# Kernel tuning notes

Hardware: AMD Instinct MI355X
Metric: run time of the kernel (lower is better)

Reference implementation:

```python
import jax, jax.numpy as jnp
import numpy as np

NEG_SLOPE = 0.2  # DenseGATConv default negative_slope


def dense_gat(x, adj, W, att_src, att_dst, bias):
    # x: [B,N,Cin], adj: [B,N,N] (self-loops already added), W: [Cin,H*C]
    B, N, _ = x.shape
    H, C = att_src.shape
    h = (x @ W).reshape(B, N, H, C)
    a_src = jnp.einsum('bnhc,hc->bnh', h, att_src)  # [B,N,H]
    a_dst = jnp.einsum('bnhc,hc->bnh', h, att_dst)
    # alpha[b,i,j,h] = a_src[b,j,h] + a_dst[b,i,h]  (softmax over j, axis=2)
    alpha = a_src[:, None, :, :] + a_dst[:, :, None, :]
    alpha = jnp.where(alpha >= 0, alpha, NEG_SLOPE * alpha)  # leaky_relu
    mask = (adj != 0)[..., None]  # [B,N,N,1]
    alpha = jax.nn.softmax(jnp.where(mask, alpha, -1e30), axis=2)
    out = jnp.einsum('bijh,bjhc->bihc', alpha, h).reshape(B, N, H * C)
    return out + bias


def setup_inputs() -> dict:
    key = jax.random.key(0)
    ks = jax.random.split(key, 8)
    B, N, D = 1, 8192, 128
    x = jax.random.normal(ks[0], (B, N, D), dtype=jnp.float32)
    adj = (jax.random.uniform(ks[1], (B, N, N)) < 0.01).astype(jnp.float32)
    idx = jnp.arange(N)
    adj = adj.at[:, idx, idx].set(1.0)  # DenseGATConv add_loop=True
    s = 1.0 / np.sqrt(D)
    lin = lambda k: jax.random.uniform(k, (D, D), minval=-s, maxval=s, dtype=jnp.float32)
    att = lambda k: jax.random.normal(k, (1, D), dtype=jnp.float32) * 0.1  # heads=1
    return dict(
        x=x, adj=adj,
        W0=lin(ks[2]), att_src0=att(ks[3]), att_dst0=att(ks[4]), b0=jnp.zeros((D,), jnp.float32),
        W1=lin(ks[5]), att_src1=att(ks[6]), att_dst1=att(ks[7]), b1=jnp.zeros((D,), jnp.float32),
    )


def reference(x, adj, W0, att_src0, att_dst0, b0, W1, att_src1, att_dst1, b1):
    out0 = dense_gat(x, adj, W0, att_src0, att_dst0, b0)
    out0 = jax.nn.relu(out0)  # relu_layers_index = [0]
    out1 = dense_gat(out0, adj, W1, att_src1, att_dst1, b1)
    # dropout_rate = 0 -> dropout is identity; squeeze batch dim as in block
    return (out0[0], out1[0])
```

## Files before the change

### kernel.cpp

```cpp
#include <hip/hip_runtime.h>

#define MAXDEG 192
#define NEG_SLOPE 0.2f
#define D 128

__device__ __forceinline__ float bf2f(unsigned short u) {
    return __uint_as_float(((unsigned)u) << 16);
}
__device__ __forceinline__ unsigned short f2bf(float f) {
    unsigned u = __float_as_uint(f);
    return (unsigned short)((u + 0x7fffu + ((u >> 16) & 1u)) >> 16);
}
__device__ __forceinline__ int is_f32(const void* adj) {
    return ((const unsigned*)adj)[0] == 0x3F800000u;
}

__device__ __forceinline__ void ell_group(
        int g, const void* __restrict__ adj, int N, int f32m,
        unsigned short* __restrict__ cols, int* __restrict__ deg,
        int* __restrict__ cnt ) {
    const int w = threadIdx.x >> 6, lane = threadIdx.x & 63;
    const int row = g * 4 + w;
    if (lane == 0) cnt[w] = 0;
    __syncthreads();
    unsigned short* crow = cols + (size_t)row * MAXDEG;
    if (f32m) {
        const float4* arow = (const float4*)((const float*)adj + (size_t)row * N);
        const int nv = N / 4;
        for (int v = lane; v < nv; v += 128) {
            float4 u0 = arow[v];
            float4 u1 = arow[v + 64];
            const unsigned* a0 = (const unsigned*)&u0;
            const unsigned* a1 = (const unsigned*)&u1;
            #pragma unroll
            for (int e = 0; e < 4; e++)
                if (a0[e]) { int p = atomicAdd(&cnt[w], 1); if (p < MAXDEG) crow[p] = (unsigned short)(v * 4 + e); }
            #pragma unroll
            for (int e = 0; e < 4; e++)
                if (a1[e]) { int p = atomicAdd(&cnt[w], 1); if (p < MAXDEG) crow[p] = (unsigned short)((v + 64) * 4 + e); }
        }
    } else {
        const uint4* arow = (const uint4*)((const unsigned short*)adj + (size_t)row * N);
        const int nv = N / 8;
        for (int v = lane; v < nv; v += 128) {
            uint4 u0 = arow[v];
            uint4 u1 = arow[v + 64];
            const unsigned short* s0 = (const unsigned short*)&u0;
            const unsigned short* s1 = (const unsigned short*)&u1;
            #pragma unroll
            for (int e = 0; e < 8; e++)
                if (s0[e]) { int p = atomicAdd(&cnt[w], 1); if (p < MAXDEG) crow[p] = (unsigned short)(v * 8 + e); }
            #pragma unroll
            for (int e = 0; e < 8; e++)
                if (s1[e]) { int p = atomicAdd(&cnt[w], 1); if (p < MAXDEG) crow[p] = (unsigned short)((v + 64) * 8 + e); }
        }
    }
    __syncthreads();
    if (lane == 0) deg[row] = cnt[w] < MAXDEG ? cnt[w] : MAXDEG;
}

__device__ __forceinline__ void gemm_tile(
        int t, const void* __restrict__ A, const void* __restrict__ W,
        int aF, int f32m, const void* __restrict__ attS, const void* __restrict__ attD,
        float* __restrict__ H, float* __restrict__ asrc, float* __restrict__ adst,
        float* __restrict__ smem) {
    float* xs = smem;
    float* ws = smem + 4096;
    const int tid = threadIdx.x;
    const size_t row0 = (size_t)t * 32;

    if (aF) {
        const float4* av = (const float4*)((const float*)A + row0 * D);
        float4* xl = (float4*)xs;
        #pragma unroll
        for (int k = 0; k < 4; k++) xl[tid + 256 * k] = av[tid + 256 * k];
    } else {
        const uint4* av = (const uint4*)((const unsigned short*)A + row0 * D);
        #pragma unroll
        for (int k = 0; k < 2; k++) {
            uint4 u = av[tid + 256 * k];
            const unsigned short* us = (const unsigned short*)&u;
            #pragma unroll
            for (int e = 0; e < 8; e++) xs[(tid + 256 * k) * 8 + e] = bf2f(us[e]);
        }
    }

    const int tx = tid & 31, ty = tid >> 5;
    const int c0 = tx * 4, r0 = ty * 4;
    float acc[4][4] = {};
    for (int p = 0; p < 4; p++) {
        __syncthreads();
        if (f32m) {
            const float4* wv = (const float4*)((const float*)W + (size_t)p * 32 * D);
            float4* wl = (float4*)ws;
            #pragma unroll
            for (int k = 0; k < 4; k++) wl[tid + 256 * k] = wv[tid + 256 * k];
        } else {
            const uint4* wv = (const uint4*)((const unsigned short*)W + (size_t)p * 32 * D);
            #pragma unroll
            for (int k = 0; k < 2; k++) {
                uint4 u = wv[tid + 256 * k];
                const unsigned short* us = (const unsigned short*)&u;
                #pragma unroll
                for (int e = 0; e < 8; e++) ws[(tid + 256 * k) * 8 + e] = bf2f(us[e]);
            }
        }
        __syncthreads();
        #pragma unroll 8
        for (int k = 0; k < 32; k++) {
            float4 wv = *(const float4*)&ws[k * D + c0];
            #pragma unroll
            for (int i = 0; i < 4; i++) {
                float xv = xs[(r0 + i) * D + p * 32 + k];
                acc[i][0] += xv * wv.x; acc[i][1] += xv * wv.y;
                acc[i][2] += xv * wv.z; acc[i][3] += xv * wv.w;
            }
        }
    }
    float* Ho = H + row0 * D;
    #pragma unroll
    for (int i = 0; i < 4; i++)
        *(float4*)&Ho[(r0 + i) * D + c0] =
            make_float4(acc[i][0], acc[i][1], acc[i][2], acc[i][3]);

    float aSv[4], aDv[4];
    #pragma unroll
    for (int j = 0; j < 4; j++) {
        aSv[j] = f32m ? ((const float*)attS)[c0 + j] : bf2f(((const unsigned short*)attS)[c0 + j]);
        aDv[j] = f32m ? ((const float*)attD)[c0 + j] : bf2f(((const unsigned short*)attD)[c0 + j]);
    }
    #pragma unroll
    for (int i = 0; i < 4; i++) {
        float s = acc[i][0] * aSv[0] + acc[i][1] * aSv[1] + acc[i][2] * aSv[2] + acc[i][3] * aSv[3];
        float d = acc[i][0] * aDv[0] + acc[i][1] * aDv[1] + acc[i][2] * aDv[2] + acc[i][3] * aDv[3];
        #pragma unroll
        for (int off = 16; off > 0; off >>= 1) {
            s += __shfl_down(s, off, 32);
            d += __shfl_down(d, off, 32);
        }
        if (tx == 0) {
            asrc[row0 + r0 + i] = s;
            adst[row0 + r0 + i] = d;
        }
    }
}

__global__ __launch_bounds__(256) void ell_gemm0(
        const void* __restrict__ x, const void* __restrict__ adj,
        const void* __restrict__ W0, const void* __restrict__ aS0,
        const void* __restrict__ aD0, int N,
        unsigned short* __restrict__ cols, int* __restrict__ deg,
        float* __restrict__ h, float* __restrict__ asrc, float* __restrict__ adst) {
    __shared__ float smem[8192];
    const int bid = blockIdx.x;
    const int f32m = is_f32(adj);
    const int GT = N / 32;
    if (bid < GT)
        gemm_tile(bid, x, W0, f32m, f32m, aS0, aD0, h, asrc, adst, smem);
    else
        ell_group(bid - GT, adj, N, f32m, cols, deg, (int*)smem);
}

__global__ __launch_bounds__(256) void aggregate(
        const float* __restrict__ H,
        const float* __restrict__ asrc, const float* __restrict__ adst,
        const unsigned short* __restrict__ cols, const int* __restrict__ deg,
        const void* __restrict__ bias, const void* __restrict__ adjFlag,
        float* __restrict__ outF, void* __restrict__ outAny,
        size_t off2, int relu) {
    __shared__ float scnA[4 * MAXDEG];
    __shared__ unsigned short sjjA[4 * MAXDEG];
    const int w = threadIdx.x >> 6, lane = threadIdx.x & 63;
    const int row = blockIdx.x * 4 + w;
    float* scn = scnA + w * MAXDEG;
    unsigned short* sjj = sjjA + w * MAXDEG;
    const int d = deg[row];
    const float ai = adst[row];
    const unsigned short* crow = cols + (size_t)row * MAXDEG;

    const int s0 = lane, s1 = lane + 64, s2 = lane + 128;
    unsigned short j0 = 0, j1 = 0, j2 = 0;
    float e0 = -3e38f, e1 = -3e38f, e2 = -3e38f;
    if (s0 < d) { j0 = crow[s0]; float e = asrc[j0] + ai; e0 = (e >= 0.f) ? e : NEG_SLOPE * e; }
    if (s1 < d) { j1 = crow[s1]; float e = asrc[j1] + ai; e1 = (e >= 0.f) ? e : NEG_SLOPE * e; }
    if (s2 < d) { j2 = crow[s2]; float e = asrc[j2] + ai; e2 = (e >= 0.f) ? e : NEG_SLOPE * e; }
    float m = fmaxf(e0, fmaxf(e1, e2));
    #pragma unroll
    for (int off = 1; off < 64; off <<= 1) m = fmaxf(m, __shfl_xor(m, off));
    float p0 = (s0 < d) ? __expf(e0 - m) : 0.f;
    float p1 = (s1 < d) ? __expf(e1 - m) : 0.f;
    float p2 = (s2 < d) ? __expf(e2 - m) : 0.f;
    float l = p0 + p1 + p2;
    #pragma unroll
    for (int off = 1; off < 64; off <<= 1) l += __shfl_xor(l, off);
    const float invl = 1.f / l;
    scn[s0] = p0 * invl; sjj[s0] = j0;
    scn[s1] = p1 * invl; sjj[s1] = j1;
    scn[s2] = p2 * invl; sjj[s2] = j2;

    const float2* H2 = (const float2*)H;
    float2 acc[8];
    #pragma unroll
    for (int u = 0; u < 8; u++) acc[u] = make_float2(0.f, 0.f);
    int k = 0;
    for (; k + 7 < d; k += 8) {
        int jj[8]; float ww[8]; float2 vv[8];
        #pragma unroll
        for (int u = 0; u < 8; u++) { jj[u] = sjj[k + u]; ww[u] = scn[k + u]; }
        #pragma unroll
        for (int u = 0; u < 8; u++) vv[u] = H2[(size_t)jj[u] * 64 + lane];
        #pragma unroll
        for (int u = 0; u < 8; u++) { acc[u].x += ww[u] * vv[u].x; acc[u].y += ww[u] * vv[u].y; }
    }
    for (; k < d; k++) {
        const int j = sjj[k];
        const float wk = scn[k];
        const float2 v = H2[(size_t)j * 64 + lane];
        acc[0].x += wk * v.x; acc[0].y += wk * v.y;
    }
    #pragma unroll
    for (int u = 1; u < 8; u++) { acc[0].x += acc[u].x; acc[0].y += acc[u].y; }
    float vx = acc[0].x, vy = acc[0].y;

    const int f32m = is_f32(adjFlag);
    const int c0 = lane * 2;
    const float bx = f32m ? ((const float*)bias)[c0]     : bf2f(((const unsigned short*)bias)[c0]);
    const float by = f32m ? ((const float*)bias)[c0 + 1] : bf2f(((const unsigned short*)bias)[c0 + 1]);
    vx += bx; vy += by;
    if (relu) { vx = fmaxf(vx, 0.f); vy = fmaxf(vy, 0.f); }
    if (outF) ((float2*)outF)[(size_t)row * 64 + lane] = make_float2(vx, vy);
    if (f32m) {
        ((float2*)outAny)[off2 + (size_t)row * 64 + lane] = make_float2(vx, vy);
    } else {
        unsigned packed = (unsigned)f2bf(vx) | ((unsigned)f2bf(vy) << 16);
        ((unsigned*)outAny)[off2 + (size_t)row * 64 + lane] = packed;
    }
}

__global__ __launch_bounds__(256) void gemm1(
        const float* __restrict__ A, const void* __restrict__ W1,
        const void* __restrict__ aS1, const void* __restrict__ aD1,
        const void* __restrict__ adjFlag,
        float* __restrict__ h, float* __restrict__ asrc, float* __restrict__ adst) {
    __shared__ float smem[8192];
    const int f32m = is_f32(adjFlag);
    gemm_tile(blockIdx.x, A, W1, 1, f32m, aS1, aD1, h, asrc, adst, smem);
}

extern "C" void kernel_launch(void* const* d_in, const int* in_sizes, int n_in,
                              void* d_out, int out_size, void* d_ws, size_t ws_size,
                              hipStream_t stream) {
    const int N = in_sizes[0] / D;

    char* w = (char*)d_ws;
    int* deg             = (int*)w;            w += (size_t)N * sizeof(int);
    unsigned short* cols = (unsigned short*)w; w += (size_t)N * MAXDEG * sizeof(unsigned short);
    float* h             = (float*)w;          w += (size_t)N * D * sizeof(float);
    float* out0          = (float*)w;          w += (size_t)N * D * sizeof(float);
    float* asrc          = (float*)w;          w += (size_t)N * sizeof(float);
    float* adst          = (float*)w;

    const void* adj = d_in[1];

    ell_gemm0<<<N / 32 + N / 4, 256, 0, stream>>>(
        d_in[0], adj, d_in[2], d_in[3], d_in[4], N, cols, deg, h, asrc, adst);

    aggregate<<<N / 4, 256, 0, stream>>>(h, asrc, adst, cols, deg, d_in[5], adj,
                                         out0, d_out, 0, 1);

    gemm1<<<N / 32, 256, 0, stream>>>(out0, d_in[6], d_in[7], d_in[8], adj,
                                      h, asrc, adst);

    aggregate<<<N / 4, 256, 0, stream>>>(h, asrc, adst, cols, deg, d_in[9], adj,
                                         nullptr, d_out, (size_t)N * (D / 2), 0);
}
```

Before: 448.8 us.

## Store hidden features in bf16 and fuse layer-0 aggregation with layer-1 GEMM

Projected features H are now written as bf16 instead of fp32, halving the bytes moved by the neighbour gathers in aggregation. The layer-0 aggregation is fused with the layer-1 linear projection: each block aggregates 8 rows into shared memory and immediately multiplies them by W1. This removes the fp32 out0 intermediate and one kernel launch. In exchange, H loses precision, and the fused GEMM uses small 8-row tiles that reload W1 for every block.

```diff
diff --git a/kernel.cpp b/kernel.cpp
--- a/kernel.cpp
+++ b/kernel.cpp
@@ -10,6 +10,9 @@
 __device__ __forceinline__ unsigned short f2bf(float f) {
     unsigned u = __float_as_uint(f);
     return (unsigned short)((u + 0x7fffu + ((u >> 16) & 1u)) >> 16);
+}
+__device__ __forceinline__ unsigned pack2bf(float x, float y) {
+    return (unsigned)f2bf(x) | ((unsigned)f2bf(y) << 16);
 }
 __device__ __forceinline__ int is_f32(const void* adj) {
     return ((const unsigned*)adj)[0] == 0x3F800000u;
@@ -59,10 +62,10 @@
     if (lane == 0) deg[row] = cnt[w] < MAXDEG ? cnt[w] : MAXDEG;
 }
 
-__device__ __forceinline__ void gemm_tile(
+__device__ __forceinline__ void gemm_tile32(
         int t, const void* __restrict__ A, const void* __restrict__ W,
         int aF, int f32m, const void* __restrict__ attS, const void* __restrict__ attD,
-        float* __restrict__ H, float* __restrict__ asrc, float* __restrict__ adst,
+        unsigned short* __restrict__ Hb, float* __restrict__ asrc, float* __restrict__ adst,
         float* __restrict__ smem) {
     float* xs = smem;
     float* ws = smem + 4096;
@@ -117,11 +120,13 @@
             }
         }
     }
-    float* Ho = H + row0 * D;
-    #pragma unroll
-    for (int i = 0; i < 4; i++)
-        *(float4*)&Ho[(r0 + i) * D + c0] =
-            make_float4(acc[i][0], acc[i][1], acc[i][2], acc[i][3]);
+    #pragma unroll
+    for (int i = 0; i < 4; i++) {
+        ushort4 hv;
+        hv.x = f2bf(acc[i][0]); hv.y = f2bf(acc[i][1]);
+        hv.z = f2bf(acc[i][2]); hv.w = f2bf(acc[i][3]);
+        *(ushort4*)&Hb[(row0 + r0 + i) * D + c0] = hv;
+    }
 
     float aSv[4], aDv[4];
     #pragma unroll
@@ -145,39 +150,12 @@
     }
 }
 
-__global__ __launch_bounds__(256) void ell_gemm0(
-        const void* __restrict__ x, const void* __restrict__ adj,
-        const void* __restrict__ W0, const void* __restrict__ aS0,
-        const void* __restrict__ aD0, int N,
-        unsigned short* __restrict__ cols, int* __restrict__ deg,
-        float* __restrict__ h, float* __restrict__ asrc, float* __restrict__ adst) {
-    __shared__ float smem[8192];
-    const int bid = blockIdx.x;
-    const int f32m = is_f32(adj);
-    const int GT = N / 32;
-    if (bid < GT)
-        gemm_tile(bid, x, W0, f32m, f32m, aS0, aD0, h, asrc, adst, smem);
-    else
-        ell_group(bid - GT, adj, N, f32m, cols, deg, (int*)smem);
-}
-
-__global__ __launch_bounds__(256) void aggregate(
-        const float* __restrict__ H,
-        const float* __restrict__ asrc, const float* __restrict__ adst,
-        const unsigned short* __restrict__ cols, const int* __restrict__ deg,
-        const void* __restrict__ bias, const void* __restrict__ adjFlag,
-        float* __restrict__ outF, void* __restrict__ outAny,
-        size_t off2, int relu) {
-    __shared__ float scnA[4 * MAXDEG];
-    __shared__ unsigned short sjjA[4 * MAXDEG];
-    const int w = threadIdx.x >> 6, lane = threadIdx.x & 63;
-    const int row = blockIdx.x * 4 + w;
-    float* scn = scnA + w * MAXDEG;
-    unsigned short* sjj = sjjA + w * MAXDEG;
-    const int d = deg[row];
-    const float ai = adst[row];
-    const unsigned short* crow = cols + (size_t)row * MAXDEG;
-
+__device__ __forceinline__ float2 agg_row_bf(
+        int row, const unsigned short* __restrict__ Hb,
+        const float* __restrict__ asrc, float ai,
+        const unsigned short* __restrict__ crow, int d,
+        const void* __restrict__ bias, int f32m, int relu,
+        float* __restrict__ scn, unsigned short* __restrict__ sjj, int lane) {
     const int s0 = lane, s1 = lane + 64, s2 = lane + 128;
     unsigned short j0 = 0, j1 = 0, j2 = 0;
     float e0 = -3e38f, e1 = -3e38f, e2 = -3e38f;
@@ -198,53 +176,159 @@
     scn[s1] = p1 * invl; sjj[s1] = j1;
     scn[s2] = p2 * invl; sjj[s2] = j2;
 
-    const float2* H2 = (const float2*)H;
-    float2 acc[8];
-    #pragma unroll
-    for (int u = 0; u < 8; u++) acc[u] = make_float2(0.f, 0.f);
+    const unsigned* H2 = (const unsigned*)Hb;
+    float ax[8], ay[8];
+    #pragma unroll
+    for (int u = 0; u < 8; u++) { ax[u] = 0.f; ay[u] = 0.f; }
     int k = 0;
     for (; k + 7 < d; k += 8) {
-        int jj[8]; float ww[8]; float2 vv[8];
+        int jj[8]; float ww[8]; unsigned vv[8];
         #pragma unroll
         for (int u = 0; u < 8; u++) { jj[u] = sjj[k + u]; ww[u] = scn[k + u]; }
         #pragma unroll
         for (int u = 0; u < 8; u++) vv[u] = H2[(size_t)jj[u] * 64 + lane];
         #pragma unroll
-        for (int u = 0; u < 8; u++) { acc[u].x += ww[u] * vv[u].x; acc[u].y += ww[u] * vv[u].y; }
+        for (int u = 0; u < 8; u++) {
+            ax[u] += ww[u] * bf2f((unsigned short)(vv[u] & 0xffff));
+            ay[u] += ww[u] * bf2f((unsigned short)(vv[u] >> 16));
+        }
     }
     for (; k < d; k++) {
         const int j = sjj[k];
         const float wk = scn[k];
-        const float2 v = H2[(size_t)j * 64 + lane];
-        acc[0].x += wk * v.x; acc[0].y += wk * v.y;
-    }
-    #pragma unroll
-    for (int u = 1; u < 8; u++) { acc[0].x += acc[u].x; acc[0].y += acc[u].y; }
-    float vx = acc[0].x, vy = acc[0].y;
-
-    const int f32m = is_f32(adjFlag);
+        unsigned v = H2[(size_t)j * 64 + lane];
+        ax[0] += wk * bf2f((unsigned short)(v & 0xffff));
+        ay[0] += wk * bf2f((unsigned short)(v >> 16));
+    }
+    #pragma unroll
+    for (int u = 1; u < 8; u++) { ax[0] += ax[u]; ay[0] += ay[u]; }
+
     const int c0 = lane * 2;
     const float bx = f32m ? ((const float*)bias)[c0]     : bf2f(((const unsigned short*)bias)[c0]);
     const float by = f32m ? ((const float*)bias)[c0 + 1] : bf2f(((const unsigned short*)bias)[c0 + 1]);
-    vx += bx; vy += by;
+    float vx = ax[0] + bx, vy = ay[0] + by;
     if (relu) { vx = fmaxf(vx, 0.f); vy = fmaxf(vy, 0.f); }
-    if (outF) ((float2*)outF)[(size_t)row * 64 + lane] = make_float2(vx, vy);
-    if (f32m) {
-        ((float2*)outAny)[off2 + (size_t)row * 64 + lane] = make_float2(vx, vy);
-    } else {
-        unsigned packed = (unsigned)f2bf(vx) | ((unsigned)f2bf(vy) << 16);
-        ((unsigned*)outAny)[off2 + (size_t)row * 64 + lane] = packed;
-    }
-}
-
-__global__ __launch_bounds__(256) void gemm1(
-        const float* __restrict__ A, const void* __restrict__ W1,
+    return make_float2(vx, vy);
+}
+
+__global__ __launch_bounds__(256) void ell_gemm0(
+        const void* __restrict__ x, const void* __restrict__ adj,
+        const void* __restrict__ W0, const void* __restrict__ aS0,
+        const void* __restrict__ aD0, int N,
+        unsigned short* __restrict__ cols, int* __restrict__ deg,
+        unsigned short* __restrict__ h, float* __restrict__ asrc, float* __restrict__ adst) {
+    __shared__ float smem[8192];
+    const int bid = blockIdx.x;
+    const int f32m = is_f32(adj);
+    const int GT = N / 32;
+    if (bid < GT)
+        gemm_tile32(bid, x, W0, f32m, f32m, aS0, aD0, h, asrc, adst, smem);
+    else
+        ell_group(bid - GT, adj, N, f32m, cols, deg, (int*)smem);
+}
+
+__global__ __launch_bounds__(256) void agg0_gemm1(
+        const unsigned short* __restrict__ h,
+        const float* __restrict__ asrc0, const float* __restrict__ adst0,
+        const unsigned short* __restrict__ cols, const int* __restrict__ deg,
+        const void* __restrict__ b0, const void* __restrict__ W1,
         const void* __restrict__ aS1, const void* __restrict__ aD1,
-        const void* __restrict__ adjFlag,
-        float* __restrict__ h, float* __restrict__ asrc, float* __restrict__ adst) {
-    __shared__ float smem[8192];
+        const void* __restrict__ adjFlag, void* __restrict__ out,
+        unsigned short* __restrict__ h2,
+        float* __restrict__ asrc1, float* __restrict__ adst1, int N) {
+    __shared__ float xs[8 * D];
+    __shared__ float wstage[32 * D];
+    __shared__ float scnA[4 * MAXDEG];
+    __shared__ unsigned short sjjA[4 * MAXDEG];
+    const int tid = threadIdx.x;
+    const int w = tid >> 6, lane = tid & 63;
     const int f32m = is_f32(adjFlag);
-    gemm_tile(blockIdx.x, A, W1, 1, f32m, aS1, aD1, h, asrc, adst, smem);
+
+    #pragma unroll
+    for (int pass = 0; pass < 2; pass++) {
+        const int rl = pass * 4 + w;
+        const int row = blockIdx.x * 8 + rl;
+        float2 v = agg_row_bf(row, h, asrc0, adst0[row],
+                              cols + (size_t)row * MAXDEG, deg[row],
+                              b0, f32m, 1,
+                              scnA + w * MAXDEG, sjjA + w * MAXDEG, lane);
+        xs[rl * D + 2 * lane]     = v.x;
+        xs[rl * D + 2 * lane + 1] = v.y;
+        if (f32m) ((float2*)out)[(size_t)row * 64 + lane] = v;
+        else      ((unsigned*)out)[(size_t)row * 64 + lane] = pack2bf(v.x, v.y);
+    }
+
+    const int tx = tid & 31, ty = tid >> 5;
+    const int c0 = tx * 4;
+    float acc[4] = {};
+    for (int p = 0; p < 4; p++) {
+        __syncthreads();
+        if (f32m) {
+            const float4* wv = (const float4*)((const float*)W1 + (size_t)p * 32 * D);
+            float4* wl = (float4*)wstage;
+            #pragma unroll
+            for (int k = 0; k < 4; k++) wl[tid + 256 * k] = wv[tid + 256 * k];
+        } else {
+            const uint4* wv = (const uint4*)((const unsigned short*)W1 + (size_t)p * 32 * D);
+            #pragma unroll
+            for (int k = 0; k < 2; k++) {
+                uint4 u = wv[tid + 256 * k];
+                const unsigned short* us = (const unsigned short*)&u;
+                #pragma unroll
+                for (int e = 0; e < 8; e++) wstage[(tid + 256 * k) * 8 + e] = bf2f(us[e]);
+            }
+        }
+        __syncthreads();
+        #pragma unroll 8
+        for (int k = 0; k < 32; k++) {
+            float4 wv = *(const float4*)&wstage[k * D + c0];
+            float xv = xs[ty * D + p * 32 + k];
+            acc[0] += xv * wv.x; acc[1] += xv * wv.y;
+            acc[2] += xv * wv.z; acc[3] += xv * wv.w;
+        }
+    }
+    const size_t row1 = (size_t)blockIdx.x * 8 + ty;
+    ushort4 hv;
+    hv.x = f2bf(acc[0]); hv.y = f2bf(acc[1]); hv.z = f2bf(acc[2]); hv.w = f2bf(acc[3]);
+    *(ushort4*)&h2[row1 * D + c0] = hv;
+
+    float aSv[4], aDv[4];
+    #pragma unroll
+    for (int j = 0; j < 4; j++) {
+        aSv[j] = f32m ? ((const float*)aS1)[c0 + j] : bf2f(((const unsigned short*)aS1)[c0 + j]);
+        aDv[j] = f32m ? ((const float*)aD1)[c0 + j] : bf2f(((const unsigned short*)aD1)[c0 + j]);
+    }
+    float s = acc[0] * aSv[0] + acc[1] * aSv[1] + acc[2] * aSv[2] + acc[3] * aSv[3];
+    float d = acc[0] * aDv[0] + acc[1] * aDv[1] + acc[2] * aDv[2] + acc[3] * aDv[3];
+    #pragma unroll
+    for (int off = 16; off > 0; off >>= 1) {
+        s += __shfl_down(s, off, 32);
+        d += __shfl_down(d, off, 32);
+    }
+    if (tx == 0) {
+        asrc1[row1] = s;
+        adst1[row1] = d;
+    }
+}
+
+__global__ __launch_bounds__(256) void aggregate1(
+        const unsigned short* __restrict__ h2,
+        const float* __restrict__ asrc1, const float* __restrict__ adst1,
+        const unsigned short* __restrict__ cols, const int* __restrict__ deg,
+        const void* __restrict__ b1, const void* __restrict__ adjFlag,
+        void* __restrict__ out, int N) {
+    __shared__ float scnA[4 * MAXDEG];
+    __shared__ unsigned short sjjA[4 * MAXDEG];
+    const int w = threadIdx.x >> 6, lane = threadIdx.x & 63;
+    const int row = blockIdx.x * 4 + w;
+    const int f32m = is_f32(adjFlag);
+    float2 v = agg_row_bf(row, h2, asrc1, adst1[row],
+                          cols + (size_t)row * MAXDEG, deg[row],
+                          b1, f32m, 0,
+                          scnA + w * MAXDEG, sjjA + w * MAXDEG, lane);
+    const size_t off2 = (size_t)N * 64;
+    if (f32m) ((float2*)out)[off2 + (size_t)row * 64 + lane] = v;
+    else      ((unsigned*)out)[off2 + (size_t)row * 64 + lane] = pack2bf(v.x, v.y);
 }
 
 extern "C" void kernel_launch(void* const* d_in, const int* in_sizes, int n_in,
@@ -255,22 +339,22 @@
     char* w = (char*)d_ws;
     int* deg             = (int*)w;            w += (size_t)N * sizeof(int);
     unsigned short* cols = (unsigned short*)w; w += (size_t)N * MAXDEG * sizeof(unsigned short);
-    float* h             = (float*)w;          w += (size_t)N * D * sizeof(float);
-    float* out0          = (float*)w;          w += (size_t)N * D * sizeof(float);
-    float* asrc          = (float*)w;          w += (size_t)N * sizeof(float);
-    float* adst          = (float*)w;
+    unsigned short* h    = (unsigned short*)w; w += (size_t)N * D * sizeof(unsigned short);
+    unsigned short* h2   = (unsigned short*)w; w += (size_t)N * D * sizeof(unsigned short);
+    float* asrc0         = (float*)w;          w += (size_t)N * sizeof(float);
+    float* adst0         = (float*)w;          w += (size_t)N * sizeof(float);
+    float* asrc1         = (float*)w;          w += (size_t)N * sizeof(float);
+    float* adst1         = (float*)w;
 
     const void* adj = d_in[1];
 
     ell_gemm0<<<N / 32 + N / 4, 256, 0, stream>>>(
-        d_in[0], adj, d_in[2], d_in[3], d_in[4], N, cols, deg, h, asrc, adst);
-
-    aggregate<<<N / 4, 256, 0, stream>>>(h, asrc, adst, cols, deg, d_in[5], adj,
-                                         out0, d_out, 0, 1);
-
-    gemm1<<<N / 32, 256, 0, stream>>>(out0, d_in[6], d_in[7], d_in[8], adj,
-                                      h, asrc, adst);
-
-    aggregate<<<N / 4, 256, 0, stream>>>(h, asrc, adst, cols, deg, d_in[9], adj,
-                                         nullptr, d_out, (size_t)N * (D / 2), 0);
-}
+        d_in[0], adj, d_in[2], d_in[3], d_in[4], N, cols, deg, h, asrc0, adst0);
+
+    agg0_gemm1<<<N / 8, 256, 0, stream>>>(
+        h, asrc0, adst0, cols, deg, d_in[5], d_in[6], d_in[7], d_in[8],
+        adj, d_out, h2, asrc1, adst1, N);
+
+    aggregate1<<<N / 4, 256, 0, stream>>>(
+        h2, asrc1, adst1, cols, deg, d_in[9], adj, d_out, N);
+}
```

New measurement: 419.1 us. -6.6%, faster.
